# Performance work log

Measured on AMD Instinct MI355X. Metric: run time of the kernel, lower is better.

Reference implementation:

```python
import jax, jax.numpy as jnp
import numpy as np

N = 20        # number_of_nodes
K = 2         # Chebyshev order
E_DIM = 4     # embedding_dimensions
OUT = 2       # out_channels
F_IN = 8      # node_features
B = 131072    # batch


def setup_inputs() -> dict:
    key = jax.random.key(0)
    ks = jax.random.split(key, 8)
    x = jax.random.normal(ks[0], (B, N, F_IN), jnp.float32)
    e = jax.random.normal(ks[1], (N, E_DIM), jnp.float32)
    # AVWGCN parameter pools: weights_pool (E_DIM, K, in, out), bias_pool (E_DIM, out)
    gate_w = jax.random.normal(ks[2], (E_DIM, K, F_IN + OUT, 2 * OUT), jnp.float32) * 0.1
    gate_b = jax.random.normal(ks[3], (E_DIM, 2 * OUT), jnp.float32) * 0.1
    upd_w = jax.random.normal(ks[4], (E_DIM, K, F_IN + OUT, OUT), jnp.float32) * 0.1
    upd_b = jax.random.normal(ks[5], (E_DIM, OUT), jnp.float32) * 0.1
    lin_w = jax.random.normal(ks[6], (1, OUT), jnp.float32) * 0.5
    lin_b = jax.random.normal(ks[7], (1,), jnp.float32) * 0.1
    return {"x": x, "e": e, "gate_w": gate_w, "gate_b": gate_b,
            "upd_w": upd_w, "upd_b": upd_b, "lin_w": lin_w, "lin_b": lin_b}


def _avwgcn(x, e, supports, w_pool, b_pool):
    # Node-adaptive weights: (N, K, in, out) and bias (N, out)
    W = jnp.einsum('nd,dkio->nkio', e, w_pool)
    b = e @ b_pool
    # K-hop graph conv gather: (B, N, K, in)
    x_g = jnp.einsum('knm,bmc->bnkc', supports, x)
    return jnp.einsum('bnki,nkio->bno', x_g, W) + b


def reference(x, e, gate_w, gate_b, upd_w, upd_b, lin_w, lin_b):
    dt = x.dtype
    # Adaptive adjacency: softmax(relu(E E^T)) rows; Chebyshev set for K=2 is [I, A]
    A = jax.nn.softmax(jax.nn.relu(e @ e.T), axis=1)
    supports = jnp.stack([jnp.eye(N, dtype=dt), A.astype(dt)])  # (K, N, N)

    H = jnp.zeros((x.shape[0], N, OUT), dt)  # self.h is None -> zeros
    XH = jnp.concatenate([x, H], axis=-1)
    ZR = jax.nn.sigmoid(_avwgcn(XH, e, supports, gate_w, gate_b))
    Z, R = ZR[..., :OUT], ZR[..., OUT:]
    C = jnp.concatenate([x, Z * H], axis=-1)
    HC = jnp.tanh(_avwgcn(C, e, supports, upd_w, upd_b))
    H = R * H + (1.0 - R) * HC

    y = jax.nn.relu(H)
    y = y @ lin_w.T + lin_b
    return y
```

## Files before the change

kernel.cpp:

```cpp
#include <hip/hip_runtime.h>
#include <math.h>

#define NN 20
#define ED 4
#define XROW 160
#define NC 80
#define NKT 5
#define NNT 5
#define FRAG_BYTES (NKT * NNT * 64 * 16)
#define SSET_OFF   FRAG_BYTES
#define EPI_ROWS 128
#define EPI_STRIDE 84
#define EPI_BYTES (EPI_ROWS * EPI_STRIDE * 4)
#define BIAS_OFF   EPI_BYTES
#define LIN_OFF    (BIAS_OFF + NC * 4)
#define SMEM_BYTES (LIN_OFF + 16)
#define THREADS 1024
#define ROWS_PER_WAVE 32
#define ROWS_PER_BLOCK 512

typedef __attribute__((ext_vector_type(8))) _Float16 half8;
typedef __attribute__((ext_vector_type(4))) float f32x4;
typedef __attribute__((ext_vector_type(4))) unsigned uint4v;

static __device__ __forceinline__ half8 cvt8(float4 a, float4 b) {
    half8 r;
    r[0] = (_Float16)a.x; r[1] = (_Float16)a.y; r[2] = (_Float16)a.z; r[3] = (_Float16)a.w;
    r[4] = (_Float16)b.x; r[5] = (_Float16)b.y; r[6] = (_Float16)b.z; r[7] = (_Float16)b.w;
    return r;
}

__global__ __launch_bounds__(THREADS, 4) void rgcn_fused(
        const float* __restrict__ x,
        const float* __restrict__ e,
        const float* __restrict__ gate_w,
        const float* __restrict__ gate_b,
        const float* __restrict__ upd_w,
        const float* __restrict__ upd_b,
        const float* __restrict__ lin_w,
        const float* __restrict__ lin_b,
        float* __restrict__ y) {
    __shared__ __align__(16) char smem[SMEM_BYTES];
    float* sset  = (float*)(smem + SSET_OFF);
    float* el    = sset;
    float* sA    = sset + 80;
    float* wself = sset + 480;
    float* wagg  = sset + 1120;
    float* sbias = (float*)(smem + BIAS_OFF);
    float* slin  = (float*)(smem + LIN_OFF);

    const int t = threadIdx.x;
    const int l = t & 63;
    const int w = t >> 6;

    const size_t row0 = (size_t)blockIdx.x * ROWS_PER_BLOCK + (size_t)w * ROWS_PER_WAVE;
    const float* xq0 = x + (row0 + (l & 15)) * XROW + ((l >> 4) << 3);
    const float* xq1 = xq0 + (size_t)16 * XROW;
    float4 pa0 = *(const float4*)(xq0);
    float4 pb0 = *(const float4*)(xq0 + 4);
    float4 pa1 = *(const float4*)(xq1);
    float4 pb1 = *(const float4*)(xq1 + 4);

    if (t < NN * ED) el[t] = e[t];
    __syncthreads();

    if (t < 400) {
        int n = t / 20, m = t - (t / 20) * 20;
        float d = 0.f;
        for (int j = 0; j < ED; ++j) d += el[n * ED + j] * el[m * ED + j];
        sA[t] = fmaxf(d, 0.f);
    }
    for (int idx = t; idx < 1280; idx += THREADS) {
        int sel = idx >= 640;
        int rem = sel ? idx - 640 : idx;
        int c = rem >> 3, i = rem & 7;
        int n = c >> 2, ro = c & 3;
        float v = 0.f;
        if (ro < 2) {
            int o = 2 + ro;
            for (int d = 0; d < ED; ++d) v += el[n * ED + d] * gate_w[d * 80 + sel * 40 + i * 4 + o];
        } else {
            int o = ro - 2;
            for (int d = 0; d < ED; ++d) v += el[n * ED + d] * upd_w[d * 40 + sel * 20 + i * 2 + o];
        }
        (sel ? wagg : wself)[rem] = v;
    }
    if (t < NC) {
        int n = t >> 2, ro = t & 3;
        float b = 0.f;
        for (int d = 0; d < ED; ++d)
            b += el[n * ED + d] * (ro < 2 ? gate_b[d * 4 + 2 + ro] : upd_b[d * 2 + ro - 2]);
        sbias[t] = b;
    }
    if (t == 0) { slin[0] = lin_w[0]; slin[1] = lin_w[1]; slin[2] = lin_b[0]; }
    __syncthreads();

    if (t < NN) {
        float mx = -1e30f;
        for (int m = 0; m < NN; ++m) mx = fmaxf(mx, sA[t * 20 + m]);
        float ex[NN]; float sum = 0.f;
        for (int m = 0; m < NN; ++m) { ex[m] = __expf(sA[t * 20 + m] - mx); sum += ex[m]; }
        float inv = 1.f / sum;
        for (int m = 0; m < NN; ++m) sA[t * 20 + m] = ex[m] * inv;
    }
    __syncthreads();

    {
        half8* frag = (half8*)smem;
        for (int tile = w; tile < NKT * NNT; tile += 16) {
            int kt = tile / 5, nt = tile - kt * 5;
            int c = nt * 16 + (l & 15);
            int n = c >> 2;
            int m = kt * 4 + (l >> 4);
            float anm = sA[n * 20 + m];
            float4 wg0 = *(const float4*)&wagg[c * 8];
            float4 wg1 = *(const float4*)&wagg[c * 8 + 4];
            float v0 = anm * wg0.x, v1 = anm * wg0.y, v2 = anm * wg0.z, v3 = anm * wg0.w;
            float v4 = anm * wg1.x, v5 = anm * wg1.y, v6 = anm * wg1.z, v7 = anm * wg1.w;
            if (n == m) {
                float4 ws0 = *(const float4*)&wself[c * 8];
                float4 ws1 = *(const float4*)&wself[c * 8 + 4];
                v0 += ws0.x; v1 += ws0.y; v2 += ws0.z; v3 += ws0.w;
                v4 += ws1.x; v5 += ws1.y; v6 += ws1.z; v7 += ws1.w;
            }
            half8 hv;
            hv[0] = (_Float16)v0; hv[1] = (_Float16)v1; hv[2] = (_Float16)v2; hv[3] = (_Float16)v3;
            hv[4] = (_Float16)v4; hv[5] = (_Float16)v5; hv[6] = (_Float16)v6; hv[7] = (_Float16)v7;
            frag[tile * 64 + l] = hv;
        }
    }
    __syncthreads();

    const half8* frag = (const half8*)smem;
    f32x4 acc[2][NNT];
    #pragma unroll
    for (int g = 0; g < 2; ++g)
        #pragma unroll
        for (int nt = 0; nt < NNT; ++nt) acc[g][nt] = (f32x4){0.f, 0.f, 0.f, 0.f};

    #pragma unroll
    for (int kt = 0; kt < NKT; ++kt) {
        float4 na0, nb0, na1, nb1;
        if (kt < NKT - 1) {
            na0 = *(const float4*)(xq0 + (kt + 1) * 32);
            nb0 = *(const float4*)(xq0 + (kt + 1) * 32 + 4);
            na1 = *(const float4*)(xq1 + (kt + 1) * 32);
            nb1 = *(const float4*)(xq1 + (kt + 1) * 32 + 4);
        }
        half8 a0 = cvt8(pa0, pb0);
        half8 a1 = cvt8(pa1, pb1);
        #pragma unroll
        for (int nt = 0; nt < NNT; ++nt) {
            half8 bh = frag[(kt * NNT + nt) * 64 + l];
            acc[0][nt] = __builtin_amdgcn_mfma_f32_16x16x32_f16(a0, bh, acc[0][nt], 0, 0, 0);
            acc[1][nt] = __builtin_amdgcn_mfma_f32_16x16x32_f16(a1, bh, acc[1][nt], 0, 0, 0);
        }
        pa0 = na0; pb0 = nb0; pa1 = na1; pb1 = nb1;
    }

    const float lw0 = slin[0], lw1 = slin[1], lb = slin[2];
    __syncthreads();
    float* epi = (float*)smem;
    #pragma unroll
    for (int mt = 0; mt < 2; ++mt) {
        #pragma unroll
        for (int qb = 0; qb < 4; qb += 2) {
            #pragma unroll
            for (int nt = 0; nt < NNT; ++nt) {
                int c = nt * 16 + (l & 15);
                float bia = sbias[c];
                #pragma unroll
                for (int dq = 0; dq < 2; ++dq) {
                    int rc = w * 8 + ((l >> 4) << 1) + dq;
                    epi[rc * EPI_STRIDE + c] = acc[mt][nt][qb + dq] + bia;
                }
            }
            __syncthreads();
            #pragma unroll
            for (int o = t; o < EPI_ROWS * NN; o += THREADS) {
                int rc = o / 20;
                int n = o - rc * 20;
                float4 p = *(const float4*)&epi[rc * EPI_STRIDE + n * 4];
                float i0 = 1.f / (1.f + __expf(p.x));
                float i1 = 1.f / (1.f + __expf(p.y));
                float t0 = 1.f - 2.f / (__expf(2.f * p.z) + 1.f);
                float t1 = 1.f - 2.f / (__expf(2.f * p.w) + 1.f);
                float h0 = i0 * t0;
                float h1 = i1 * t1;
                float yv = fmaxf(h0, 0.f) * lw0 + fmaxf(h1, 0.f) * lw1 + lb;
                size_t g = (size_t)blockIdx.x * ROWS_PER_BLOCK
                         + (size_t)(rc >> 3) * ROWS_PER_WAVE
                         + (size_t)mt * 16 + (((rc & 7) >> 1) << 2) + qb + (rc & 1);
                y[g * NN + n] = yv;
            }
            __syncthreads();
        }
    }
}

extern "C" void kernel_launch(void* const* d_in, const int* in_sizes, int n_in,
                              void* d_out, int out_size, void* d_ws, size_t ws_size,
                              hipStream_t stream) {
    const float* x      = (const float*)d_in[0];
    const float* e      = (const float*)d_in[1];
    const float* gate_w = (const float*)d_in[2];
    const float* gate_b = (const float*)d_in[3];
    const float* upd_w  = (const float*)d_in[4];
    const float* upd_b  = (const float*)d_in[5];
    const float* lin_w  = (const float*)d_in[6];
    const float* lin_b  = (const float*)d_in[7];
    float* y = (float*)d_out;

    const int Bn = in_sizes[0] / XROW;
    const int nblocks = Bn / ROWS_PER_BLOCK;

    rgcn_fused<<<nblocks, THREADS, 0, stream>>>(x, e, gate_w, gate_b,
                                                upd_w, upd_b, lin_w, lin_b, y);
}
```

Measured before the change: 30.40 us.

## Split weight setup into a one-block prologue kernel and shrink main blocks

Moves the per-block softmax adjacency and adaptive weight fragment construction into a single-block setup kernel that writes fp16 MFMA fragments, bias and linear params to workspace. The main kernel then just copies these into LDS. The main kernel also uses 512-thread blocks of 128 rows with one 16-row tile per wave and issues all five x loads up front. The epilogue switches to hardware reciprocal. This removes redundant setup work from every block and improves occupancy, at the cost of an extra kernel launch and a serial dependency between the two kernels.

```diff
diff --git a/kernel.cpp b/kernel.cpp
--- a/kernel.cpp
+++ b/kernel.cpp
@@ -8,16 +8,14 @@
 #define NKT 5
 #define NNT 5
 #define FRAG_BYTES (NKT * NNT * 64 * 16)
-#define SSET_OFF   FRAG_BYTES
-#define EPI_ROWS 128
+#define BIAS_OFF   FRAG_BYTES
+#define LIN_OFF    (BIAS_OFF + NC * 4)
+#define CONS_BYTES (LIN_OFF + 16)
+#define CONS_U4    (CONS_BYTES / 16)
+#define THREADS 512
+#define ROWS_PER_WAVE 16
+#define ROWS_PER_BLOCK 128
 #define EPI_STRIDE 84
-#define EPI_BYTES (EPI_ROWS * EPI_STRIDE * 4)
-#define BIAS_OFF   EPI_BYTES
-#define LIN_OFF    (BIAS_OFF + NC * 4)
-#define SMEM_BYTES (LIN_OFF + 16)
-#define THREADS 1024
-#define ROWS_PER_WAVE 32
-#define ROWS_PER_BLOCK 512
 
 typedef __attribute__((ext_vector_type(8))) _Float16 half8;
 typedef __attribute__((ext_vector_type(4))) float f32x4;
@@ -30,36 +28,21 @@
     return r;
 }
 
-__global__ __launch_bounds__(THREADS, 4) void rgcn_fused(
-        const float* __restrict__ x,
-        const float* __restrict__ e,
-        const float* __restrict__ gate_w,
-        const float* __restrict__ gate_b,
-        const float* __restrict__ upd_w,
-        const float* __restrict__ upd_b,
-        const float* __restrict__ lin_w,
-        const float* __restrict__ lin_b,
-        float* __restrict__ y) {
-    __shared__ __align__(16) char smem[SMEM_BYTES];
-    float* sset  = (float*)(smem + SSET_OFF);
-    float* el    = sset;
-    float* sA    = sset + 80;
-    float* wself = sset + 480;
-    float* wagg  = sset + 1120;
-    float* sbias = (float*)(smem + BIAS_OFF);
-    float* slin  = (float*)(smem + LIN_OFF);
-
+__global__ void rgcn_setup(const float* __restrict__ e,
+                           const float* __restrict__ gate_w,
+                           const float* __restrict__ gate_b,
+                           const float* __restrict__ upd_w,
+                           const float* __restrict__ upd_b,
+                           const float* __restrict__ lin_w,
+                           const float* __restrict__ lin_b,
+                           char* __restrict__ ws) {
+    __shared__ float el[80];
+    __shared__ float sA[400];
+    __shared__ float wself[640];
+    __shared__ float wagg[640];
     const int t = threadIdx.x;
     const int l = t & 63;
     const int w = t >> 6;
-
-    const size_t row0 = (size_t)blockIdx.x * ROWS_PER_BLOCK + (size_t)w * ROWS_PER_WAVE;
-    const float* xq0 = x + (row0 + (l & 15)) * XROW + ((l >> 4) << 3);
-    const float* xq1 = xq0 + (size_t)16 * XROW;
-    float4 pa0 = *(const float4*)(xq0);
-    float4 pb0 = *(const float4*)(xq0 + 4);
-    float4 pa1 = *(const float4*)(xq1);
-    float4 pb1 = *(const float4*)(xq1 + 4);
 
     if (t < NN * ED) el[t] = e[t];
     __syncthreads();
@@ -85,14 +68,16 @@
         }
         (sel ? wagg : wself)[rem] = v;
     }
+    float* wbias = (float*)(ws + BIAS_OFF);
+    float* wlin  = (float*)(ws + LIN_OFF);
     if (t < NC) {
         int n = t >> 2, ro = t & 3;
         float b = 0.f;
         for (int d = 0; d < ED; ++d)
             b += el[n * ED + d] * (ro < 2 ? gate_b[d * 4 + 2 + ro] : upd_b[d * 2 + ro - 2]);
-        sbias[t] = b;
-    }
-    if (t == 0) { slin[0] = lin_w[0]; slin[1] = lin_w[1]; slin[2] = lin_b[0]; }
+        wbias[t] = b;
+    }
+    if (t == 0) { wlin[0] = lin_w[0]; wlin[1] = lin_w[1]; wlin[2] = lin_b[0]; wlin[3] = 0.f; }
     __syncthreads();
 
     if (t < NN) {
@@ -105,96 +90,115 @@
     }
     __syncthreads();
 
+    half8* frag = (half8*)ws;
+    for (int tile = w; tile < NKT * NNT; tile += (THREADS / 64)) {
+        int kt = tile / 5, nt = tile - kt * 5;
+        int c = nt * 16 + (l & 15);
+        int n = c >> 2;
+        int m = kt * 4 + (l >> 4);
+        float anm = sA[n * 20 + m];
+        float4 wg0 = *(const float4*)&wagg[c * 8];
+        float4 wg1 = *(const float4*)&wagg[c * 8 + 4];
+        float v0 = anm * wg0.x, v1 = anm * wg0.y, v2 = anm * wg0.z, v3 = anm * wg0.w;
+        float v4 = anm * wg1.x, v5 = anm * wg1.y, v6 = anm * wg1.z, v7 = anm * wg1.w;
+        if (n == m) {
+            float4 ws0 = *(const float4*)&wself[c * 8];
+            float4 ws1 = *(const float4*)&wself[c * 8 + 4];
+            v0 += ws0.x; v1 += ws0.y; v2 += ws0.z; v3 += ws0.w;
+            v4 += ws1.x; v5 += ws1.y; v6 += ws1.z; v7 += ws1.w;
+        }
+        half8 hv;
+        hv[0] = (_Float16)v0; hv[1] = (_Float16)v1; hv[2] = (_Float16)v2; hv[3] = (_Float16)v3;
+        hv[4] = (_Float16)v4; hv[5] = (_Float16)v5; hv[6] = (_Float16)v6; hv[7] = (_Float16)v7;
+        frag[tile * 64 + l] = hv;
+    }
+}
+
+__global__ __launch_bounds__(THREADS, 6) void rgcn_main(
+        const float* __restrict__ x,
+        const char* __restrict__ cons,
+        float* __restrict__ y) {
+    __shared__ __align__(16) char smem[CONS_BYTES];
+    const int t = threadIdx.x;
+    const int l = t & 63;
+    const int w = t >> 6;
+
+    const size_t row0 = (size_t)blockIdx.x * ROWS_PER_BLOCK + (size_t)w * ROWS_PER_WAVE;
+    const float* xp = x + (row0 + (l & 15)) * XROW + ((l >> 4) << 3);
+    float4 xa0 = *(const float4*)(xp);       float4 xb0 = *(const float4*)(xp + 4);
+    float4 xa1 = *(const float4*)(xp + 32);  float4 xb1 = *(const float4*)(xp + 36);
+    float4 xa2 = *(const float4*)(xp + 64);  float4 xb2 = *(const float4*)(xp + 68);
+    float4 xa3 = *(const float4*)(xp + 96);  float4 xb3 = *(const float4*)(xp + 100);
+    float4 xa4 = *(const float4*)(xp + 128); float4 xb4 = *(const float4*)(xp + 132);
+
     {
-        half8* frag = (half8*)smem;
-        for (int tile = w; tile < NKT * NNT; tile += 16) {
-            int kt = tile / 5, nt = tile - kt * 5;
-            int c = nt * 16 + (l & 15);
-            int n = c >> 2;
-            int m = kt * 4 + (l >> 4);
-            float anm = sA[n * 20 + m];
-            float4 wg0 = *(const float4*)&wagg[c * 8];
-            float4 wg1 = *(const float4*)&wagg[c * 8 + 4];
-            float v0 = anm * wg0.x, v1 = anm * wg0.y, v2 = anm * wg0.z, v3 = anm * wg0.w;
-            float v4 = anm * wg1.x, v5 = anm * wg1.y, v6 = anm * wg1.z, v7 = anm * wg1.w;
-            if (n == m) {
-                float4 ws0 = *(const float4*)&wself[c * 8];
-                float4 ws1 = *(const float4*)&wself[c * 8 + 4];
-                v0 += ws0.x; v1 += ws0.y; v2 += ws0.z; v3 += ws0.w;
-                v4 += ws1.x; v5 += ws1.y; v6 += ws1.z; v7 += ws1.w;
-            }
-            half8 hv;
-            hv[0] = (_Float16)v0; hv[1] = (_Float16)v1; hv[2] = (_Float16)v2; hv[3] = (_Float16)v3;
-            hv[4] = (_Float16)v4; hv[5] = (_Float16)v5; hv[6] = (_Float16)v6; hv[7] = (_Float16)v7;
-            frag[tile * 64 + l] = hv;
-        }
+        const uint4v* src = (const uint4v*)cons;
+        uint4v* dst = (uint4v*)smem;
+        #pragma unroll
+        for (int i = t; i < CONS_U4; i += THREADS) dst[i] = src[i];
     }
     __syncthreads();
 
     const half8* frag = (const half8*)smem;
-    f32x4 acc[2][NNT];
+    const float* sbias = (const float*)(smem + BIAS_OFF);
+    const float* slin  = (const float*)(smem + LIN_OFF);
+
+    f32x4 acc[NNT];
     #pragma unroll
-    for (int g = 0; g < 2; ++g)
-        #pragma unroll
-        for (int nt = 0; nt < NNT; ++nt) acc[g][nt] = (f32x4){0.f, 0.f, 0.f, 0.f};
-
+    for (int nt = 0; nt < NNT; ++nt) acc[nt] = (f32x4){0.f, 0.f, 0.f, 0.f};
+
+    #define STEP(XA, XB, KT)                                                        \
+    {                                                                               \
+        half8 a = cvt8(XA, XB);                                                     \
+        _Pragma("unroll")                                                           \
+        for (int nt = 0; nt < NNT; ++nt) {                                          \
+            half8 bh = frag[((KT) * NNT + nt) * 64 + l];                            \
+            acc[nt] = __builtin_amdgcn_mfma_f32_16x16x32_f16(a, bh, acc[nt], 0, 0, 0); \
+        }                                                                           \
+    }
+    STEP(xa0, xb0, 0)
+    STEP(xa1, xb1, 1)
+    STEP(xa2, xb2, 2)
+    STEP(xa3, xb3, 3)
+    STEP(xa4, xb4, 4)
+    #undef STEP
+
+    const float lw0 = slin[0], lw1 = slin[1], lb = slin[2];
+    __syncthreads();
+    float* epi = (float*)smem;
     #pragma unroll
-    for (int kt = 0; kt < NKT; ++kt) {
-        float4 na0, nb0, na1, nb1;
-        if (kt < NKT - 1) {
-            na0 = *(const float4*)(xq0 + (kt + 1) * 32);
-            nb0 = *(const float4*)(xq0 + (kt + 1) * 32 + 4);
-            na1 = *(const float4*)(xq1 + (kt + 1) * 32);
-            nb1 = *(const float4*)(xq1 + (kt + 1) * 32 + 4);
-        }
-        half8 a0 = cvt8(pa0, pb0);
-        half8 a1 = cvt8(pa1, pb1);
+    for (int qb = 0; qb < 4; qb += 2) {
         #pragma unroll
         for (int nt = 0; nt < NNT; ++nt) {
-            half8 bh = frag[(kt * NNT + nt) * 64 + l];
-            acc[0][nt] = __builtin_amdgcn_mfma_f32_16x16x32_f16(a0, bh, acc[0][nt], 0, 0, 0);
-            acc[1][nt] = __builtin_amdgcn_mfma_f32_16x16x32_f16(a1, bh, acc[1][nt], 0, 0, 0);
-        }
-        pa0 = na0; pb0 = nb0; pa1 = na1; pb1 = nb1;
-    }
-
-    const float lw0 = slin[0], lw1 = slin[1], lb = slin[2];
-    __syncthreads();
-    float* epi = (float*)smem;
-    #pragma unroll
-    for (int mt = 0; mt < 2; ++mt) {
+            int c = nt * 16 + (l & 15);
+            float bia = sbias[c];
+            #pragma unroll
+            for (int dq = 0; dq < 2; ++dq) {
+                int rc = w * 8 + ((l >> 4) << 1) + dq;
+                epi[rc * EPI_STRIDE + c] = acc[nt][qb + dq] + bia;
+            }
+        }
+        __syncthreads();
         #pragma unroll
-        for (int qb = 0; qb < 4; qb += 2) {
-            #pragma unroll
-            for (int nt = 0; nt < NNT; ++nt) {
-                int c = nt * 16 + (l & 15);
-                float bia = sbias[c];
-                #pragma unroll
-                for (int dq = 0; dq < 2; ++dq) {
-                    int rc = w * 8 + ((l >> 4) << 1) + dq;
-                    epi[rc * EPI_STRIDE + c] = acc[mt][nt][qb + dq] + bia;
-                }
-            }
-            __syncthreads();
-            #pragma unroll
-            for (int o = t; o < EPI_ROWS * NN; o += THREADS) {
-                int rc = o / 20;
-                int n = o - rc * 20;
-                float4 p = *(const float4*)&epi[rc * EPI_STRIDE + n * 4];
-                float i0 = 1.f / (1.f + __expf(p.x));
-                float i1 = 1.f / (1.f + __expf(p.y));
-                float t0 = 1.f - 2.f / (__expf(2.f * p.z) + 1.f);
-                float t1 = 1.f - 2.f / (__expf(2.f * p.w) + 1.f);
-                float h0 = i0 * t0;
-                float h1 = i1 * t1;
-                float yv = fmaxf(h0, 0.f) * lw0 + fmaxf(h1, 0.f) * lw1 + lb;
-                size_t g = (size_t)blockIdx.x * ROWS_PER_BLOCK
-                         + (size_t)(rc >> 3) * ROWS_PER_WAVE
-                         + (size_t)mt * 16 + (((rc & 7) >> 1) << 2) + qb + (rc & 1);
-                y[g * NN + n] = yv;
-            }
-            __syncthreads();
-        }
+        for (int o = t; o < 64 * NN; o += THREADS) {
+            int rc = o / 20;
+            int n = o - rc * 20;
+            float4 p = *(const float4*)&epi[rc * EPI_STRIDE + n * 4];
+            float e0 = __expf(p.x);
+            float e1 = __expf(p.y);
+            float i0 = __builtin_amdgcn_rcpf(1.f + e0);
+            float i1 = __builtin_amdgcn_rcpf(1.f + e1);
+            float t0 = 1.f - 2.f * __builtin_amdgcn_rcpf(__expf(2.f * p.z) + 1.f);
+            float t1 = 1.f - 2.f * __builtin_amdgcn_rcpf(__expf(2.f * p.w) + 1.f);
+            float h0 = i0 * t0;
+            float h1 = i1 * t1;
+            float yv = fmaxf(h0, 0.f) * lw0 + fmaxf(h1, 0.f) * lw1 + lb;
+            size_t g = (size_t)blockIdx.x * ROWS_PER_BLOCK
+                     + (size_t)(rc >> 3) * ROWS_PER_WAVE
+                     + (((rc & 7) >> 1) << 2) + qb + (rc & 1);
+            y[g * NN + n] = yv;
+        }
+        __syncthreads();
     }
 }
 
@@ -209,11 +213,13 @@
     const float* upd_b  = (const float*)d_in[5];
     const float* lin_w  = (const float*)d_in[6];
     const float* lin_b  = (const float*)d_in[7];
-    float* y = (float*)d_out;
+    char* cons = (char*)d_ws;
+    float* y   = (float*)d_out;
 
     const int Bn = in_sizes[0] / XROW;
     const int nblocks = Bn / ROWS_PER_BLOCK;
 
-    rgcn_fused<<<nblocks, THREADS, 0, stream>>>(x, e, gate_w, gate_b,
-                                                upd_w, upd_b, lin_w, lin_b, y);
-}
+    rgcn_setup<<<1, THREADS, 0, stream>>>(e, gate_w, gate_b, upd_w, upd_b,
+                                          lin_w, lin_b, cons);
+    rgcn_main<<<nblocks, THREADS, 0, stream>>>(x, cons, y);
+}
```

Result: faster. 26.18 us (-13.9%).
